# Kernel tuning notes

Hardware: AMD Instinct MI355X
Metric: run time of the kernel (lower is better)

Reference implementation:

```python
import jax, jax.numpy as jnp
import numpy as np

N = 100000       # num_nodes
E = 800000       # num edges (avg degree 8)
EMB = 64         # emb_dim
HID = 256        # hidden_dim


def setup_inputs() -> dict:
    key = jax.random.key(0)
    k1, k2, k3, k4, k5, k6, k7 = jax.random.split(key, 7)
    def xavier(k, fan_in, fan_out):
        limit = float(np.sqrt(6.0 / (fan_in + fan_out)))
        return jax.random.uniform(k, (fan_in, fan_out), jnp.float32, -limit, limit)
    return {
        "row": jax.random.randint(k1, (E,), 0, N, dtype=jnp.int64) if jax.config.jax_enable_x64 else jax.random.randint(k1, (E,), 0, N).astype(jnp.int32),
        "col": jax.random.randint(k2, (E,), 0, N).astype(jnp.int32),
        "val": jax.random.uniform(k3, (E,), jnp.float32),
        "emb": jax.random.normal(k4, (N, EMB), jnp.float32) * 0.02,
        "W0": xavier(k5, EMB, HID),
        "W1": xavier(k6, HID, HID),
        "W2": xavier(k7, HID, HID),
    }


def reference(row, col, val, emb, W0, W1, W2):
    # SpMM: out[r] = sum_{edges e with row[e]==r} val[e] * emb[col[e]]
    msgs = val[:, None] * emb[col]                      # [E, EMB] gather + scale
    x = jax.ops.segment_sum(msgs, row, num_segments=N)  # [N, EMB] scatter-add
    # MLP (bias-free linears; dropout=0.0 / eval mode => identity)
    x = jax.nn.relu(x @ W0)   # [N, HID]
    x = jax.nn.relu(x @ W1)   # [N, HID]
    x = x @ W2                # [N, HID]
    return x
```

## Files before the change

### kernel.cpp

```cpp
#include <hip/hip_runtime.h>
#include <hip/hip_bf16.h>

#define EMB 64
#define HID 256

typedef __attribute__((ext_vector_type(8))) short short8_t;
typedef __attribute__((ext_vector_type(4))) float f32x4;

__device__ __forceinline__ unsigned short f2bf(float f)
{
    union { float f; unsigned int u; } c; c.f = f;
    unsigned int u = c.u;
    u += 0x7fffu + ((u >> 16) & 1u);
    return (unsigned short)(u >> 16);
}
__device__ __forceinline__ float bf2f(unsigned short b)
{
    union { unsigned int u; float f; } c; c.u = ((unsigned int)b) << 16;
    return c.f;
}

__global__ __launch_bounds__(256) void prep_kernel(
    const float* __restrict__ emb, const float* __restrict__ W0,
    const float* __restrict__ W1, const float* __restrict__ W2,
    int* __restrict__ counts, unsigned short* __restrict__ embb,
    unsigned short* __restrict__ W0f, unsigned short* __restrict__ W1f,
    unsigned short* __restrict__ W2f, int M, int zb, int cb)
{
    int b = blockIdx.x;
    if (b < zb) {
        int idx = (b * 256 + threadIdx.x) * 4;
        if (idx + 3 < M) {
            int4 z; z.x = 0; z.y = 0; z.z = 0; z.w = 0;
            *(int4*)&counts[idx] = z;
        } else {
            for (int i = idx; i < M; ++i) counts[i] = 0;
        }
        return;
    }
    b -= zb;
    if (b < cb) {
        int idx = (b * 256 + threadIdx.x) * 4;
        if (idx + 3 < M * EMB) {
            float4 v = *(const float4*)&emb[idx];
            ushort4 o;
            o.x = f2bf(v.x); o.y = f2bf(v.y); o.z = f2bf(v.z); o.w = f2bf(v.w);
            *(ushort4*)&embb[idx] = o;
        }
        return;
    }
    b -= cb;
    if (b < 8) {
        int i    = b * 256 + threadIdx.x;
        int lane = i & 63;
        int kc   = (i >> 6) & 1;
        int nt   = i >> 7;
        int lr   = lane & 15, kg = lane >> 4;
        unsigned short tmp[8];
#pragma unroll
        for (int j = 0; j < 8; ++j)
            tmp[j] = f2bf(W0[(kc * 32 + kg * 8 + j) * HID + nt * 16 + lr]);
        *(short8_t*)&W0f[(size_t)i * 8] = *(short8_t*)tmp;
        return;
    }
    b -= 8;
    if (b < 32) {
        int i    = b * 256 + threadIdx.x;
        int lane = i & 63;
        int kc   = (i >> 6) & 7;
        int nt   = i >> 9;
        int lr   = lane & 15, kg = lane >> 4;
        unsigned short tmp[8];
#pragma unroll
        for (int j = 0; j < 8; ++j)
            tmp[j] = f2bf(W1[(kc * 32 + kg * 8 + j) * HID + nt * 16 + lr]);
        *(short8_t*)&W1f[(size_t)i * 8] = *(short8_t*)tmp;
        return;
    }
    b -= 32;
    {
        int i    = b * 256 + threadIdx.x;
        int lane = i & 63;
        int kc   = (i >> 6) & 7;
        int nt   = i >> 9;
        int lr   = lane & 15, kg = lane >> 4;
        unsigned short tmp[8];
#pragma unroll
        for (int j = 0; j < 8; ++j)
            tmp[j] = f2bf(W2[(kc * 32 + kg * 8 + j) * HID + nt * 16 + lr]);
        *(short8_t*)&W2f[(size_t)i * 8] = *(short8_t*)tmp;
    }
}

__global__ __launch_bounds__(256) void hist_kernel(
    const int* __restrict__ row, int* __restrict__ counts, int E)
{
    int base = (blockIdx.x * 256 + threadIdx.x) * 4;
    if (base + 3 < E) {
        int4 r4 = *(const int4*)&row[base];
        atomicAdd(&counts[r4.x], 1);
        atomicAdd(&counts[r4.y], 1);
        atomicAdd(&counts[r4.z], 1);
        atomicAdd(&counts[r4.w], 1);
    } else {
        for (int i = base; i < E; ++i) atomicAdd(&counts[row[i]], 1);
    }
}

__global__ __launch_bounds__(256) void scan_phase1(
    const int* __restrict__ counts, int* __restrict__ excl,
    int* __restrict__ blockSums, int n)
{
    __shared__ int s[256];
    int t = threadIdx.x;
    int base = blockIdx.x * 1024 + t * 4;
    int4 v = {0, 0, 0, 0};
    if (base + 3 < n) {
        v = *(const int4*)&counts[base];
    } else {
        if (base + 0 < n) v.x = counts[base + 0];
        if (base + 1 < n) v.y = counts[base + 1];
        if (base + 2 < n) v.z = counts[base + 2];
        if (base + 3 < n) v.w = counts[base + 3];
    }
    int tsum = v.x + v.y + v.z + v.w;
    s[t] = tsum;
    __syncthreads();
#pragma unroll
    for (int off = 1; off < 256; off <<= 1) {
        int val = (t >= off) ? s[t - off] : 0;
        __syncthreads();
        s[t] += val;
        __syncthreads();
    }
    if (t == 255) blockSums[blockIdx.x] = s[255];
    int e0 = s[t] - tsum;
    int e1 = e0 + v.x;
    int e2 = e1 + v.y;
    int e3 = e2 + v.z;
    if (base + 0 < n) excl[base + 0] = e0;
    if (base + 1 < n) excl[base + 1] = e1;
    if (base + 2 < n) excl[base + 2] = e2;
    if (base + 3 < n) excl[base + 3] = e3;
}

__global__ __launch_bounds__(256) void scan_phase2(int* blockSums, int nb)
{
    __shared__ int s[256];
    int t = threadIdx.x;
    int v = (t < nb) ? blockSums[t] : 0;
    s[t] = v;
    __syncthreads();
#pragma unroll
    for (int off = 1; off < 256; off <<= 1) {
        int val = (t >= off) ? s[t - off] : 0;
        __syncthreads();
        s[t] += val;
        __syncthreads();
    }
    if (t < nb) blockSums[t] = s[t] - v;
}

__global__ __launch_bounds__(256) void scan_phase3(
    int* __restrict__ offsets, const int* __restrict__ blockSums,
    int* __restrict__ cursor, int n)
{
    int i = blockIdx.x * 256 + threadIdx.x;
    if (i >= n) return;
    int o = offsets[i] + blockSums[i >> 10];
    offsets[i] = o;
    cursor[i]  = o;
}

__global__ __launch_bounds__(256) void scatter_kernel(
    const int* __restrict__ row, const int* __restrict__ col,
    const float* __restrict__ val, int* __restrict__ cursor,
    uint2* __restrict__ edata, int E)
{
    int e = blockIdx.x * 256 + threadIdx.x;
    if (e >= E) return;
    int r = row[e];
    int pos = atomicAdd(&cursor[r], 1);
    uint2 d;
    d.x = (unsigned)col[e];
    d.y = __float_as_uint(val[e]);
    edata[pos] = d;
}

#define ROWS_PER_WAVE 8
__global__ __launch_bounds__(256) void pull_kernel(
    const int* __restrict__ offsets, const int* __restrict__ counts,
    const uint2* __restrict__ edata, const unsigned short* __restrict__ embb,
    unsigned short* __restrict__ xb, int Nn)
{
    const int nw   = gridDim.x * 4;
    const int wid  = blockIdx.x * 4 + (threadIdx.x >> 6);
    const int lane = threadIdx.x & 63;
    if (wid >= Nn) return;

    int beg = offsets[wid];
    int cnt = counts[wid];
    for (int r = wid; r < Nn; r += nw) {
        int rn = r + nw;
        int begN = 0, cntN = 0;
        if (rn < Nn) { begN = offsets[rn]; cntN = counts[rn]; }

        float acc = 0.f;
        for (int i = 0; i < cnt; i += 8) {
            uint2 ed[8];
#pragma unroll
            for (int j = 0; j < 8; ++j) {
                int idx = i + j;
                idx = (idx < cnt) ? idx : (cnt - 1);
                ed[j] = edata[beg + idx];
            }
            float g[8];
#pragma unroll
            for (int j = 0; j < 8; ++j)
                g[j] = bf2f(embb[(size_t)ed[j].x * EMB + lane]);
#pragma unroll
            for (int j = 0; j < 8; ++j) {
                float v = (i + j < cnt) ? __uint_as_float(ed[j].y) : 0.f;
                acc += v * g[j];
            }
        }
        xb[(size_t)r * EMB + lane] = f2bf(acc);
        beg = begN; cnt = cntN;
    }
}

__global__ __launch_bounds__(256) void mlp_fused(
    const unsigned short* __restrict__ xb,
    const unsigned short* __restrict__ W0f,
    const unsigned short* __restrict__ W1f,
    const unsigned short* __restrict__ W2f,
    float* __restrict__ out, int M)
{
    __shared__ unsigned short H[32 * 256];

    const int t    = threadIdx.x;
    const int lane = t & 63;
    const int w    = t >> 6;
    const int lr   = lane & 15;
    const int kg   = lane >> 4;
    const int row0 = blockIdx.x * 32;
    char* Hb = (char*)H;

#define HOFF(row, bytecol) ((((row) * 512) + (bytecol)) ^ (((row) & 7) << 4))

    short8_t ax[2][2];
#pragma unroll
    for (int kc = 0; kc < 2; ++kc)
#pragma unroll
        for (int m = 0; m < 2; ++m) {
            int gr = row0 + m * 16 + lr;
            ax[kc][m] = *(const short8_t*)(xb + (size_t)(gr < M ? gr : 0) * EMB
                                           + kc * 32 + kg * 8);
        }
    f32x4 acc[2][4] = {};
#pragma unroll
    for (int kc = 0; kc < 2; ++kc) {
        short8_t b[4];
#pragma unroll
        for (int n = 0; n < 4; ++n)
            b[n] = *(const short8_t*)&W0f[(size_t)(((w * 4 + n) * 2 + kc) * 64 + lane) * 8];
#pragma unroll
        for (int m = 0; m < 2; ++m)
#pragma unroll
            for (int n = 0; n < 4; ++n)
                acc[m][n] = __builtin_amdgcn_mfma_f32_16x16x32_bf16(
                    ax[kc][m], b[n], acc[m][n], 0, 0, 0);
    }
#pragma unroll
    for (int m = 0; m < 2; ++m)
#pragma unroll
        for (int r = 0; r < 4; ++r)
#pragma unroll
            for (int n = 0; n < 4; ++n)
                *(unsigned short*)(Hb + HOFF(m * 16 + kg * 4 + r,
                                             (w * 64 + n * 16 + lr) * 2)) =
                    f2bf(fmaxf(acc[m][n][r], 0.f));
    __syncthreads();

    f32x4 acc2[2][4] = {};
#pragma unroll
    for (int kc = 0; kc < 8; ++kc) {
        short8_t a[2], b[4];
#pragma unroll
        for (int n = 0; n < 4; ++n)
            b[n] = *(const short8_t*)&W1f[(size_t)(((w * 4 + n) * 8 + kc) * 64 + lane) * 8];
#pragma unroll
        for (int m = 0; m < 2; ++m)
            a[m] = *(const short8_t*)(Hb + HOFF(m * 16 + lr, kc * 64 + kg * 16));
#pragma unroll
        for (int m = 0; m < 2; ++m)
#pragma unroll
            for (int n = 0; n < 4; ++n)
                acc2[m][n] = __builtin_amdgcn_mfma_f32_16x16x32_bf16(
                    a[m], b[n], acc2[m][n], 0, 0, 0);
    }
    __syncthreads();
#pragma unroll
    for (int m = 0; m < 2; ++m)
#pragma unroll
        for (int r = 0; r < 4; ++r)
#pragma unroll
            for (int n = 0; n < 4; ++n)
                *(unsigned short*)(Hb + HOFF(m * 16 + kg * 4 + r,
                                             (w * 64 + n * 16 + lr) * 2)) =
                    f2bf(fmaxf(acc2[m][n][r], 0.f));
    __syncthreads();

    f32x4 acc3[2][4] = {};
#pragma unroll
    for (int kc = 0; kc < 8; ++kc) {
        short8_t a[2], b[4];
#pragma unroll
        for (int n = 0; n < 4; ++n)
            b[n] = *(const short8_t*)&W2f[(size_t)(((w * 4 + n) * 8 + kc) * 64 + lane) * 8];
#pragma unroll
        for (int m = 0; m < 2; ++m)
            a[m] = *(const short8_t*)(Hb + HOFF(m * 16 + lr, kc * 64 + kg * 16));
#pragma unroll
        for (int m = 0; m < 2; ++m)
#pragma unroll
            for (int n = 0; n < 4; ++n)
                acc3[m][n] = __builtin_amdgcn_mfma_f32_16x16x32_bf16(
                    a[m], b[n], acc3[m][n], 0, 0, 0);
    }
    __syncthreads();

    float* Hf = (float*)H;
#pragma unroll
    for (int m = 0; m < 2; ++m) {
#pragma unroll
        for (int n = 0; n < 4; ++n)
#pragma unroll
            for (int r = 0; r < 4; ++r)
                Hf[w * 1024 + (kg * 4 + r) * 64 + n * 16 + lr] = acc3[m][n][r];
#pragma unroll
        for (int p = 0; p < 4; ++p) {
            int rl = (lane >> 4) + p * 4;
            f32x4 v = *(const f32x4*)&Hf[w * 1024 + rl * 64 + (lane & 15) * 4];
            int gr = row0 + m * 16 + rl;
            if (gr < M)
                *(f32x4*)&out[(size_t)gr * HID + w * 64 + (lane & 15) * 4] = v;
        }
    }
#undef HOFF
}

__global__ __launch_bounds__(256) void spmm_kernel(
    const int* __restrict__ row, const int* __restrict__ col,
    const float* __restrict__ val, const float* __restrict__ emb,
    float* __restrict__ x, int E)
{
    int gid  = blockIdx.x * blockDim.x + threadIdx.x;
    int e    = gid >> 6;
    int lane = gid & 63;
    if (e >= E) return;
    unsafeAtomicAdd(&x[(size_t)row[e] * EMB + lane],
                    val[e] * emb[(size_t)col[e] * EMB + lane]);
}

template<int K, bool RELU>
__global__ __launch_bounds__(256) void gemm_f32(
    const float* A, const float* __restrict__ B, float* C, int M)
{
    __shared__ float As[64][17];
    __shared__ float Bs[16][256];

    const int t    = threadIdx.x;
    const int tn   = t & 15;
    const int row0 = blockIdx.x * 64;
    const int sk = t & 15;
    const int sm = (t >> 4) * 4;

    float acc[4][16];
#pragma unroll
    for (int i = 0; i < 4; ++i)
#pragma unroll
        for (int j = 0; j < 16; ++j) acc[i][j] = 0.f;

    const int mB = ((t & 63) >> 4) * 4;
    const int wq = t >> 6;
    const int myM = (wq * 16) + mB;

    for (int k0 = 0; k0 < K; k0 += 16) {
        __syncthreads();
#pragma unroll
        for (int i = 0; i < 4; ++i) {
            int m  = sm + i;
            int gr = row0 + m;
            As[m][sk] = (gr < M) ? A[(size_t)gr * K + k0 + sk] : 0.f;
        }
#pragma unroll
        for (int r = 0; r < 16; ++r)
            Bs[r][t] = B[(size_t)(k0 + r) * 256 + t];
        __syncthreads();

#pragma unroll
        for (int kk = 0; kk < 16; ++kk) {
            float a0 = As[myM + 0][kk];
            float a1 = As[myM + 1][kk];
            float a2 = As[myM + 2][kk];
            float a3 = As[myM + 3][kk];
            float4 b[4];
#pragma unroll
            for (int j = 0; j < 4; ++j)
                b[j] = *(const float4*)&Bs[kk][tn * 4 + j * 64];
#pragma unroll
            for (int j = 0; j < 4; ++j) {
                acc[0][j*4+0] += a0 * b[j].x;  acc[0][j*4+1] += a0 * b[j].y;
                acc[0][j*4+2] += a0 * b[j].z;  acc[0][j*4+3] += a0 * b[j].w;
                acc[1][j*4+0] += a1 * b[j].x;  acc[1][j*4+1] += a1 * b[j].y;
                acc[1][j*4+2] += a1 * b[j].z;  acc[1][j*4+3] += a1 * b[j].w;
                acc[2][j*4+0] += a2 * b[j].x;  acc[2][j*4+1] += a2 * b[j].y;
                acc[2][j*4+2] += a2 * b[j].z;  acc[2][j*4+3] += a2 * b[j].w;
                acc[3][j*4+0] += a3 * b[j].x;  acc[3][j*4+1] += a3 * b[j].y;
                acc[3][j*4+2] += a3 * b[j].z;  acc[3][j*4+3] += a3 * b[j].w;
            }
        }
    }

#pragma unroll
    for (int i = 0; i < 4; ++i) {
        int gr = row0 + myM + i;
        if (gr < M) {
#pragma unroll
            for (int j = 0; j < 4; ++j) {
                float4 o;
                o.x = acc[i][j*4+0]; o.y = acc[i][j*4+1];
                o.z = acc[i][j*4+2]; o.w = acc[i][j*4+3];
                if (RELU) {
                    o.x = fmaxf(o.x, 0.f); o.y = fmaxf(o.y, 0.f);
                    o.z = fmaxf(o.z, 0.f); o.w = fmaxf(o.w, 0.f);
                }
                *(float4*)&C[(size_t)gr * 256 + tn * 4 + j * 64] = o;
            }
        }
    }
}

extern "C" void kernel_launch(void* const* d_in, const int* in_sizes, int n_in,
                              void* d_out, int out_size, void* d_ws, size_t ws_size,
                              hipStream_t stream)
{
    const int*   row = (const int*)d_in[0];
    const int*   col = (const int*)d_in[1];
    const float* val = (const float*)d_in[2];
    const float* emb = (const float*)d_in[3];
    const float* W0  = (const float*)d_in[4];
    const float* W1  = (const float*)d_in[5];
    const float* W2  = (const float*)d_in[6];
    float* out = (float*)d_out;

    const int E = in_sizes[0];
    const int M = in_sizes[3] / EMB;

    char* ws = (char*)d_ws;

    size_t off = 0;
    auto alloc = [&](size_t bytes) { size_t o = off; off = (off + bytes + 255) & ~(size_t)255; return o; };
    const size_t off_counts = alloc((size_t)M * 4);
    const size_t off_offs   = alloc((size_t)M * 4);
    const size_t off_cursor = alloc((size_t)M * 4);
    const size_t off_bsums  = alloc(1024);
    const size_t off_edata  = alloc((size_t)E * 8);
    const size_t off_embb   = alloc((size_t)M * EMB * 2);
    const size_t off_xb     = alloc((size_t)M * EMB * 2);
    const size_t off_w0     = alloc((size_t)EMB * HID * 2);
    const size_t off_w1     = alloc((size_t)HID * HID * 2);
    const size_t off_w2     = alloc((size_t)HID * HID * 2);
    const size_t need       = off;

    if (ws_size >= need) {
        int*   counts = (int*)(ws + off_counts);
        int*   offs   = (int*)(ws + off_offs);
        int*   cursor = (int*)(ws + off_cursor);
        int*   bsums  = (int*)(ws + off_bsums);
        uint2* edata  = (uint2*)(ws + off_edata);
        unsigned short* embb = (unsigned short*)(ws + off_embb);
        unsigned short* xb  = (unsigned short*)(ws + off_xb);
        unsigned short* W0f = (unsigned short*)(ws + off_w0);
        unsigned short* W1f = (unsigned short*)(ws + off_w1);
        unsigned short* W2f = (unsigned short*)(ws + off_w2);

        int zb = (M / 4 + 255) / 256;
        int cb = ((M * EMB) / 4 + 255) / 256;
        int prep_blocks = zb + cb + 8 + 32 + 32;
        prep_kernel<<<prep_blocks, 256, 0, stream>>>(
            emb, W0, W1, W2, counts, embb, W0f, W1f, W2f, M, zb, cb);

        hist_kernel<<<(E / 4 + 255) / 256, 256, 0, stream>>>(row, counts, E);
        int nb = (M + 1023) / 1024;
        scan_phase1<<<nb, 256, 0, stream>>>(counts, offs, bsums, M);
        scan_phase2<<<1, 256, 0, stream>>>(bsums, nb);
        scan_phase3<<<(M + 255) / 256, 256, 0, stream>>>(offs, bsums, cursor, M);
        scatter_kernel<<<(E + 255) / 256, 256, 0, stream>>>(row, col, val, cursor, edata, E);

        int pull_blocks = (M + 4 * ROWS_PER_WAVE - 1) / (4 * ROWS_PER_WAVE);
        pull_kernel<<<pull_blocks, 256, 0, stream>>>(offs, counts, edata, embb, xb, M);

        int gblocks = (M + 31) / 32;
        mlp_fused<<<gblocks, 256, 0, stream>>>(xb, W0f, W1f, W2f, out, M);
    } else {
        float* x = (float*)ws;
        (void)hipMemsetAsync(x, 0, (size_t)M * EMB * sizeof(float), stream);
        spmm_kernel<<<(E + 3) / 4, 256, 0, stream>>>(row, col, val, emb, x, E);
        int gblocks = (M + 63) / 64;
        gemm_f32<EMB, true ><<<gblocks, 256, 0, stream>>>(x,   W0, out, M);
        gemm_f32<HID, true ><<<gblocks, 256, 0, stream>>>(out, W1, out, M);
        gemm_f32<HID, false><<<gblocks, 256, 0, stream>>>(out, W2, out, M);
    }
}
```

Before: 195.9 us.

## Fuse SpMM pull aggregation into the MLP kernel via shared memory

After: 212.6 us. +8.5%, slower.

```diff
diff --git a/kernel.cpp b/kernel.cpp
--- a/kernel.cpp
+++ b/kernel.cpp
@@ -187,56 +187,16 @@
     edata[pos] = d;
 }
 
-#define ROWS_PER_WAVE 8
-__global__ __launch_bounds__(256) void pull_kernel(
+__global__ __launch_bounds__(256) void mlp_fused(
     const int* __restrict__ offsets, const int* __restrict__ counts,
     const uint2* __restrict__ edata, const unsigned short* __restrict__ embb,
-    unsigned short* __restrict__ xb, int Nn)
-{
-    const int nw   = gridDim.x * 4;
-    const int wid  = blockIdx.x * 4 + (threadIdx.x >> 6);
-    const int lane = threadIdx.x & 63;
-    if (wid >= Nn) return;
-
-    int beg = offsets[wid];
-    int cnt = counts[wid];
-    for (int r = wid; r < Nn; r += nw) {
-        int rn = r + nw;
-        int begN = 0, cntN = 0;
-        if (rn < Nn) { begN = offsets[rn]; cntN = counts[rn]; }
-
-        float acc = 0.f;
-        for (int i = 0; i < cnt; i += 8) {
-            uint2 ed[8];
-#pragma unroll
-            for (int j = 0; j < 8; ++j) {
-                int idx = i + j;
-                idx = (idx < cnt) ? idx : (cnt - 1);
-                ed[j] = edata[beg + idx];
-            }
-            float g[8];
-#pragma unroll
-            for (int j = 0; j < 8; ++j)
-                g[j] = bf2f(embb[(size_t)ed[j].x * EMB + lane]);
-#pragma unroll
-            for (int j = 0; j < 8; ++j) {
-                float v = (i + j < cnt) ? __uint_as_float(ed[j].y) : 0.f;
-                acc += v * g[j];
-            }
-        }
-        xb[(size_t)r * EMB + lane] = f2bf(acc);
-        beg = begN; cnt = cntN;
-    }
-}
-
-__global__ __launch_bounds__(256) void mlp_fused(
-    const unsigned short* __restrict__ xb,
     const unsigned short* __restrict__ W0f,
     const unsigned short* __restrict__ W1f,
     const unsigned short* __restrict__ W2f,
     float* __restrict__ out, int M)
 {
     __shared__ unsigned short H[32 * 256];
+    __shared__ unsigned short X[32 * 64];
 
     const int t    = threadIdx.x;
     const int lane = t & 63;
@@ -245,17 +205,49 @@
     const int kg   = lane >> 4;
     const int row0 = blockIdx.x * 32;
     char* Hb = (char*)H;
+    char* Xb = (char*)X;
 
 #define HOFF(row, bytecol) ((((row) * 512) + (bytecol)) ^ (((row) & 7) << 4))
+#define XOFF(row, bytecol) ((((row) * 128) + (bytecol)) ^ (((row) & 7) << 4))
+
+#pragma unroll 1
+    for (int rr = 0; rr < 8; ++rr) {
+        int rloc = w * 8 + rr;
+        int r = row0 + rloc;
+        float acc = 0.f;
+        if (r < M) {
+            int beg = offsets[r];
+            int cnt = counts[r];
+            for (int i = 0; i < cnt; i += 8) {
+                uint2 ed[8];
+#pragma unroll
+                for (int j = 0; j < 8; ++j) {
+                    int idx = i + j;
+                    idx = (idx < cnt) ? idx : (cnt - 1);
+                    ed[j] = edata[beg + idx];
+                }
+                float g[8];
+#pragma unroll
+                for (int j = 0; j < 8; ++j)
+                    g[j] = bf2f(embb[(size_t)ed[j].x * EMB + lane]);
+#pragma unroll
+                for (int j = 0; j < 8; ++j) {
+                    float v = (i + j < cnt) ? __uint_as_float(ed[j].y) : 0.f;
+                    acc += v * g[j];
+                }
+            }
+        }
+        *(unsigned short*)(Xb + XOFF(rloc, lane * 2)) = f2bf(acc);
+    }
+    __syncthreads();
 
     short8_t ax[2][2];
 #pragma unroll
     for (int kc = 0; kc < 2; ++kc)
 #pragma unroll
         for (int m = 0; m < 2; ++m) {
-            int gr = row0 + m * 16 + lr;
-            ax[kc][m] = *(const short8_t*)(xb + (size_t)(gr < M ? gr : 0) * EMB
-                                           + kc * 32 + kg * 8);
+            int row = m * 16 + lr;
+            ax[kc][m] = *(const short8_t*)(Xb + XOFF(row, (kc * 32 + kg * 8) * 2));
         }
     f32x4 acc[2][4] = {};
 #pragma unroll
@@ -348,6 +340,7 @@
         }
     }
 #undef HOFF
+#undef XOFF
 }
 
 __global__ __launch_bounds__(256) void spmm_kernel(
@@ -468,7 +461,6 @@
     const size_t off_bsums  = alloc(1024);
     const size_t off_edata  = alloc((size_t)E * 8);
     const size_t off_embb   = alloc((size_t)M * EMB * 2);
-    const size_t off_xb     = alloc((size_t)M * EMB * 2);
     const size_t off_w0     = alloc((size_t)EMB * HID * 2);
     const size_t off_w1     = alloc((size_t)HID * HID * 2);
     const size_t off_w2     = alloc((size_t)HID * HID * 2);
@@ -481,7 +473,6 @@
         int*   bsums  = (int*)(ws + off_bsums);
         uint2* edata  = (uint2*)(ws + off_edata);
         unsigned short* embb = (unsigned short*)(ws + off_embb);
-        unsigned short* xb  = (unsigned short*)(ws + off_xb);
         unsigned short* W0f = (unsigned short*)(ws + off_w0);
         unsigned short* W1f = (unsigned short*)(ws + off_w1);
         unsigned short* W2f = (unsigned short*)(ws + off_w2);
@@ -499,11 +490,9 @@
         scan_phase3<<<(M + 255) / 256, 256, 0, stream>>>(offs, bsums, cursor, M);
         scatter_kernel<<<(E + 255) / 256, 256, 0, stream>>>(row, col, val, cursor, edata, E);
 
-        int pull_blocks = (M + 4 * ROWS_PER_WAVE - 1) / (4 * ROWS_PER_WAVE);
-        pull_kernel<<<pull_blocks, 256, 0, stream>>>(offs, counts, edata, embb, xb, M);
-
         int gblocks = (M + 31) / 32;
-        mlp_fused<<<gblocks, 256, 0, stream>>>(xb, W0f, W1f, W2f, out, M);
+        mlp_fused<<<gblocks, 256, 0, stream>>>(
+            offs, counts, edata, embb, W0f, W1f, W2f, out, M);
     } else {
         float* x = (float*)ws;
         (void)hipMemsetAsync(x, 0, (size_t)M * EMB * sizeof(float), stream);
```

## Prefetch MLP weight fragments two k-steps ahead and scalarize row offsets

Applied to the files above, without the earlier changes.

Result: no change. 194.8 us (-0.6%).

```diff
diff --git a/kernel.cpp b/kernel.cpp
--- a/kernel.cpp
+++ b/kernel.cpp
@@ -198,12 +198,15 @@
     const int lane = threadIdx.x & 63;
     if (wid >= Nn) return;
 
-    int beg = offsets[wid];
-    int cnt = counts[wid];
+    int beg = __builtin_amdgcn_readfirstlane(offsets[wid]);
+    int cnt = __builtin_amdgcn_readfirstlane(counts[wid]);
     for (int r = wid; r < Nn; r += nw) {
         int rn = r + nw;
         int begN = 0, cntN = 0;
-        if (rn < Nn) { begN = offsets[rn]; cntN = counts[rn]; }
+        if (rn < Nn) {
+            begN = __builtin_amdgcn_readfirstlane(offsets[rn]);
+            cntN = __builtin_amdgcn_readfirstlane(counts[rn]);
+        }
 
         float acc = 0.f;
         for (int i = 0; i < cnt; i += 8) {
@@ -271,6 +274,14 @@
                 acc[m][n] = __builtin_amdgcn_mfma_f32_16x16x32_bf16(
                     ax[kc][m], b[n], acc[m][n], 0, 0, 0);
     }
+
+    short8_t pb[2][4];
+#pragma unroll
+    for (int n = 0; n < 4; ++n) {
+        pb[0][n] = *(const short8_t*)&W1f[(size_t)(((w * 4 + n) * 8 + 0) * 64 + lane) * 8];
+        pb[1][n] = *(const short8_t*)&W1f[(size_t)(((w * 4 + n) * 8 + 1) * 64 + lane) * 8];
+    }
+
 #pragma unroll
     for (int m = 0; m < 2; ++m)
 #pragma unroll
@@ -285,10 +296,19 @@
     f32x4 acc2[2][4] = {};
 #pragma unroll
     for (int kc = 0; kc < 8; ++kc) {
-        short8_t a[2], b[4];
-#pragma unroll
-        for (int n = 0; n < 4; ++n)
-            b[n] = *(const short8_t*)&W1f[(size_t)(((w * 4 + n) * 8 + kc) * 64 + lane) * 8];
+        short8_t b[4];
+#pragma unroll
+        for (int n = 0; n < 4; ++n) b[n] = pb[kc & 1][n];
+#pragma unroll
+        for (int n = 0; n < 4; ++n) {
+            if (kc < 6)
+                pb[kc & 1][n] = *(const short8_t*)
+                    &W1f[(size_t)(((w * 4 + n) * 8 + kc + 2) * 64 + lane) * 8];
+            else
+                pb[kc & 1][n] = *(const short8_t*)
+                    &W2f[(size_t)(((w * 4 + n) * 8 + (kc - 6)) * 64 + lane) * 8];
+        }
+        short8_t a[2];
 #pragma unroll
         for (int m = 0; m < 2; ++m)
             a[m] = *(const short8_t*)(Hb + HOFF(m * 16 + lr, kc * 64 + kg * 16));
@@ -314,10 +334,16 @@
     f32x4 acc3[2][4] = {};
 #pragma unroll
     for (int kc = 0; kc < 8; ++kc) {
-        short8_t a[2], b[4];
-#pragma unroll
-        for (int n = 0; n < 4; ++n)
-            b[n] = *(const short8_t*)&W2f[(size_t)(((w * 4 + n) * 8 + kc) * 64 + lane) * 8];
+        short8_t b[4];
+#pragma unroll
+        for (int n = 0; n < 4; ++n) b[n] = pb[kc & 1][n];
+#pragma unroll
+        for (int n = 0; n < 4; ++n) {
+            if (kc < 6)
+                pb[kc & 1][n] = *(const short8_t*)
+                    &W2f[(size_t)(((w * 4 + n) * 8 + kc + 2) * 64 + lane) * 8];
+        }
+        short8_t a[2];
 #pragma unroll
         for (int m = 0; m < 2; ++m)
             a[m] = *(const short8_t*)(Hb + HOFF(m * 16 + lr, kc * 64 + kg * 16));
```
